# Kernel tuning notes

Hardware: AMD Instinct MI355X
Metric: run time of the kernel (lower is better)

The kernel has to match this reference:

```python
import jax, jax.numpy as jnp
import numpy as np

SQRT_2_OVER_PI = 0.7978845608028654
GELU_COEFF = 0.044715

def _gelu_tanh(v):
    inner = SQRT_2_OVER_PI * (v + GELU_COEFF * v * v * v)
    return 0.5 * v * (1.0 + jnp.tanh(inner))

def setup_inputs() -> dict:
    key = jax.random.key(0)
    k1, k2, k3, k4 = jax.random.split(key, 4)
    M, K, N = 16384, 4096, 4096
    x = jax.random.normal(k1, (M, K), dtype=jnp.float32)
    bound_w = np.sqrt(6.0 / K) / np.sqrt(1.0 + 5.0)  # kaiming_uniform a=sqrt(5)
    weight = jax.random.uniform(k2, (K, N), dtype=jnp.float32, minval=-bound_w, maxval=bound_w)
    bound_b = 1.0 / np.sqrt(K)
    bias = jax.random.uniform(k3, (N,), dtype=jnp.float32, minval=-bound_b, maxval=bound_b)
    subtract = jax.random.normal(k4, (N,), dtype=jnp.float32)
    return {"x": x, "weight": weight, "bias": bias, "subtract": subtract}

def reference(x, weight, bias, subtract):
    # mean_n(xW + b - s) = (x . colsum(W) + sum(b) - sum(s)) / N
    N = weight.shape[1]
    c = weight.sum(axis=1)                       # (K,)
    scale = 1.0 / N
    bias_term = (bias.sum() - subtract.sum()) * scale
    row_scalars = _gelu_tanh(x @ c * scale + bias_term)  # (M,)
    return x + row_scalars[:, None]
```

## Files before the change

### kernel.cpp

```cpp
#include <hip/hip_runtime.h>
#include <math.h>

#define K_DIM 4096
#define N_DIM 4096

__global__ void __launch_bounds__(256) colsum_kernel(const float* __restrict__ W,
                                                     float* __restrict__ c) {
    const int k = blockIdx.x;
    const float4* row = reinterpret_cast<const float4*>(W + (size_t)k * N_DIM);
    const int t = threadIdx.x;
    float acc = 0.f;
#pragma unroll
    for (int i = 0; i < N_DIM / 4 / 256; ++i) {
        float4 v = row[t + i * 256];
        acc += (v.x + v.y) + (v.z + v.w);
    }
#pragma unroll
    for (int off = 32; off > 0; off >>= 1) acc += __shfl_down(acc, off, 64);
    __shared__ float s[4];
    const int wave = t >> 6, lane = t & 63;
    if (lane == 0) s[wave] = acc;
    __syncthreads();
    if (t == 0) c[k] = (s[0] + s[1]) + (s[2] + s[3]);
}

__global__ void __launch_bounds__(256) biassum_kernel(const float* __restrict__ bias,
                                                      const float* __restrict__ subtract,
                                                      float* __restrict__ bterm) {
    const int t = threadIdx.x;
    float acc = 0.f;
    for (int i = t; i < N_DIM; i += 256) acc += bias[i] - subtract[i];
#pragma unroll
    for (int off = 32; off > 0; off >>= 1) acc += __shfl_down(acc, off, 64);
    __shared__ float s[4];
    const int wave = t >> 6, lane = t & 63;
    if (lane == 0) s[wave] = acc;
    __syncthreads();
    if (t == 0) bterm[0] = ((s[0] + s[1]) + (s[2] + s[3])) * (1.0f / (float)N_DIM);
}

__global__ void __launch_bounds__(256) rowfuse_kernel(const float* __restrict__ x,
                                                      const float* __restrict__ c,
                                                      const float* __restrict__ bterm,
                                                      float* __restrict__ out) {
    const int m = blockIdx.x;
    const float4* xr = reinterpret_cast<const float4*>(x + (size_t)m * K_DIM);
    float4* orow = reinterpret_cast<float4*>(out + (size_t)m * K_DIM);
    const float4* c4 = reinterpret_cast<const float4*>(c);
    const int t = threadIdx.x;

    float4 xv[4];
    float acc = 0.f;
#pragma unroll
    for (int i = 0; i < 4; ++i) {
        xv[i] = xr[t + i * 256];
        float4 cv = c4[t + i * 256];
        acc += xv[i].x * cv.x + xv[i].y * cv.y + xv[i].z * cv.z + xv[i].w * cv.w;
    }
#pragma unroll
    for (int off = 32; off > 0; off >>= 1) acc += __shfl_down(acc, off, 64);

    __shared__ float s[4];
    __shared__ float sg;
    const int wave = t >> 6, lane = t & 63;
    if (lane == 0) s[wave] = acc;
    __syncthreads();
    if (t == 0) {
        float d = ((s[0] + s[1]) + (s[2] + s[3])) * (1.0f / (float)N_DIM) + bterm[0];
        float inner = 0.7978845608028654f * (d + 0.044715f * d * d * d);
        sg = 0.5f * d * (1.0f + tanhf(inner));
    }
    __syncthreads();
    const float g = sg;
#pragma unroll
    for (int i = 0; i < 4; ++i) {
        float4 o = xv[i];
        o.x += g; o.y += g; o.z += g; o.w += g;
        orow[t + i * 256] = o;
    }
}

extern "C" void kernel_launch(void* const* d_in, const int* in_sizes, int n_in,
                              void* d_out, int out_size, void* d_ws, size_t ws_size,
                              hipStream_t stream) {
    const float* x        = (const float*)d_in[0];
    const float* W        = (const float*)d_in[1];
    const float* bias     = (const float*)d_in[2];
    const float* subtract = (const float*)d_in[3];
    float* out = (float*)d_out;

    float* c     = (float*)d_ws;
    float* bterm = c + K_DIM;

    const int M = in_sizes[0] / K_DIM;

    colsum_kernel<<<K_DIM, 256, 0, stream>>>(W, c);
    biassum_kernel<<<1, 256, 0, stream>>>(bias, subtract, bterm);
    rowfuse_kernel<<<M, 256, 0, stream>>>(x, c, bterm, out);
}
```

Baseline: 120.3 us.

## Merge bias-sum into colsum kernel and process multiple rows per block with prefetch

Folds the bias/subtract reduction into an extra block of the colsum kernel, which removes one launch. The row kernel now handles 8 rows per block: it loads c once into registers, prefetches the next row's x while reducing the current one, and uses xor shuffles so every thread computes GELU itself, dropping the second barrier. It also swaps tanhf for an exp-based form and writes the output with nontemporal stores. The trade-offs are more register pressure, fewer blocks, and a shared-memory array indexed per row with only one barrier per row, where correctness relies on each row having its own slot.

```diff
diff --git a/kernel.cpp b/kernel.cpp
--- a/kernel.cpp
+++ b/kernel.cpp
@@ -3,80 +3,101 @@
 
 #define K_DIM 4096
 #define N_DIM 4096
+#define ROWS_PER_BLOCK 8
+
+typedef float f32x4 __attribute__((ext_vector_type(4)));
 
 __global__ void __launch_bounds__(256) colsum_kernel(const float* __restrict__ W,
-                                                     float* __restrict__ c) {
-    const int k = blockIdx.x;
-    const float4* row = reinterpret_cast<const float4*>(W + (size_t)k * N_DIM);
+                                                     const float* __restrict__ bias,
+                                                     const float* __restrict__ subtract,
+                                                     float* __restrict__ c,
+                                                     float* __restrict__ bterm) {
     const int t = threadIdx.x;
-    float acc = 0.f;
-#pragma unroll
-    for (int i = 0; i < N_DIM / 4 / 256; ++i) {
-        float4 v = row[t + i * 256];
-        acc += (v.x + v.y) + (v.z + v.w);
-    }
-#pragma unroll
-    for (int off = 32; off > 0; off >>= 1) acc += __shfl_down(acc, off, 64);
     __shared__ float s[4];
     const int wave = t >> 6, lane = t & 63;
-    if (lane == 0) s[wave] = acc;
-    __syncthreads();
-    if (t == 0) c[k] = (s[0] + s[1]) + (s[2] + s[3]);
-}
 
-__global__ void __launch_bounds__(256) biassum_kernel(const float* __restrict__ bias,
-                                                      const float* __restrict__ subtract,
-                                                      float* __restrict__ bterm) {
-    const int t = threadIdx.x;
-    float acc = 0.f;
-    for (int i = t; i < N_DIM; i += 256) acc += bias[i] - subtract[i];
+    if (blockIdx.x < K_DIM) {
+        const int k = blockIdx.x;
+        const float4* row = reinterpret_cast<const float4*>(W + (size_t)k * N_DIM);
+        float acc = 0.f;
 #pragma unroll
-    for (int off = 32; off > 0; off >>= 1) acc += __shfl_down(acc, off, 64);
-    __shared__ float s[4];
-    const int wave = t >> 6, lane = t & 63;
-    if (lane == 0) s[wave] = acc;
-    __syncthreads();
-    if (t == 0) bterm[0] = ((s[0] + s[1]) + (s[2] + s[3])) * (1.0f / (float)N_DIM);
+        for (int i = 0; i < N_DIM / 4 / 256; ++i) {
+            float4 v = row[t + i * 256];
+            acc += (v.x + v.y) + (v.z + v.w);
+        }
+#pragma unroll
+        for (int off = 32; off > 0; off >>= 1) acc += __shfl_down(acc, off, 64);
+        if (lane == 0) s[wave] = acc;
+        __syncthreads();
+        if (t == 0) c[k] = (s[0] + s[1]) + (s[2] + s[3]);
+    } else {
+        float acc = 0.f;
+        for (int i = t; i < N_DIM; i += 256) acc += bias[i] - subtract[i];
+#pragma unroll
+        for (int off = 32; off > 0; off >>= 1) acc += __shfl_down(acc, off, 64);
+        if (lane == 0) s[wave] = acc;
+        __syncthreads();
+        if (t == 0) bterm[0] = ((s[0] + s[1]) + (s[2] + s[3])) * (1.0f / (float)N_DIM);
+    }
 }
 
 __global__ void __launch_bounds__(256) rowfuse_kernel(const float* __restrict__ x,
                                                       const float* __restrict__ c,
                                                       const float* __restrict__ bterm,
-                                                      float* __restrict__ out) {
-    const int m = blockIdx.x;
-    const float4* xr = reinterpret_cast<const float4*>(x + (size_t)m * K_DIM);
-    float4* orow = reinterpret_cast<float4*>(out + (size_t)m * K_DIM);
+                                                      float* __restrict__ out,
+                                                      int M) {
+    const int t = threadIdx.x;
+    const int row0 = blockIdx.x * ROWS_PER_BLOCK;
+
     const float4* c4 = reinterpret_cast<const float4*>(c);
-    const int t = threadIdx.x;
+    float4 cv[4];
+#pragma unroll
+    for (int i = 0; i < 4; ++i) cv[i] = c4[t + i * 256];
+    const float bt = bterm[0];
 
-    float4 xv[4];
-    float acc = 0.f;
+    const float4* xr = reinterpret_cast<const float4*>(x) + (size_t)row0 * (K_DIM / 4);
+    f32x4* orow      = reinterpret_cast<f32x4*>(out)      + (size_t)row0 * (K_DIM / 4);
+
+    __shared__ float s[ROWS_PER_BLOCK][4];
+    const int wave = t >> 6, lane = t & 63;
+
+    float4 xv[2][4];
 #pragma unroll
-    for (int i = 0; i < 4; ++i) {
-        xv[i] = xr[t + i * 256];
-        float4 cv = c4[t + i * 256];
-        acc += xv[i].x * cv.x + xv[i].y * cv.y + xv[i].z * cv.z + xv[i].w * cv.w;
-    }
+    for (int i = 0; i < 4; ++i) xv[0][i] = xr[t + i * 256];
+
 #pragma unroll
-    for (int off = 32; off > 0; off >>= 1) acc += __shfl_down(acc, off, 64);
+    for (int r = 0; r < ROWS_PER_BLOCK; ++r) {
+        const int cur = r & 1, nxt = cur ^ 1;
+        if (r + 1 < ROWS_PER_BLOCK) {
+#pragma unroll
+            for (int i = 0; i < 4; ++i)
+                xv[nxt][i] = xr[(size_t)(r + 1) * (K_DIM / 4) + t + i * 256];
+        }
+        float acc = 0.f;
+#pragma unroll
+        for (int i = 0; i < 4; ++i)
+            acc += xv[cur][i].x * cv[i].x + xv[cur][i].y * cv[i].y
+                 + xv[cur][i].z * cv[i].z + xv[cur][i].w * cv[i].w;
+#pragma unroll
+        for (int off = 32; off > 0; off >>= 1) acc += __shfl_xor(acc, off, 64);
+        if (lane == 0) s[r][wave] = acc;
+        __syncthreads();
 
-    __shared__ float s[4];
-    __shared__ float sg;
-    const int wave = t >> 6, lane = t & 63;
-    if (lane == 0) s[wave] = acc;
-    __syncthreads();
-    if (t == 0) {
-        float d = ((s[0] + s[1]) + (s[2] + s[3])) * (1.0f / (float)N_DIM) + bterm[0];
+        float d = ((s[r][0] + s[r][1]) + (s[r][2] + s[r][3])) * (1.0f / (float)N_DIM) + bt;
         float inner = 0.7978845608028654f * (d + 0.044715f * d * d * d);
-        sg = 0.5f * d * (1.0f + tanhf(inner));
-    }
-    __syncthreads();
-    const float g = sg;
+        float e  = __expf(2.0f * inner);
+        float th = 1.0f - 2.0f / (e + 1.0f);
+        float g  = 0.5f * d * (1.0f + th);
+
 #pragma unroll
-    for (int i = 0; i < 4; ++i) {
-        float4 o = xv[i];
-        o.x += g; o.y += g; o.z += g; o.w += g;
-        orow[t + i * 256] = o;
+        for (int i = 0; i < 4; ++i) {
+            f32x4 o;
+            o.x = xv[cur][i].x + g;
+            o.y = xv[cur][i].y + g;
+            o.z = xv[cur][i].z + g;
+            o.w = xv[cur][i].w + g;
+            __builtin_nontemporal_store(o, &orow[(size_t)r * (K_DIM / 4) + t + i * 256]);
+        }
     }
 }
 
@@ -94,7 +115,6 @@
 
     const int M = in_sizes[0] / K_DIM;
 
-    colsum_kernel<<<K_DIM, 256, 0, stream>>>(W, c);
-    biassum_kernel<<<1, 256, 0, stream>>>(bias, subtract, bterm);
-    rowfuse_kernel<<<M, 256, 0, stream>>>(x, c, bterm, out);
+    colsum_kernel<<<K_DIM + 1, 256, 0, stream>>>(W, bias, subtract, c, bterm);
+    rowfuse_kernel<<<M / ROWS_PER_BLOCK, 256, 0, stream>>>(x, c, bterm, out, M);
 }
```

Result: no change. 122.2 us (+1.6%).

## Merge bias-sum into colsum kernel and process one row per wave

Applied to the files above, without the earlier changes.

The bias/subtract reduction moves into an extra block of the column-sum kernel, which removes one kernel launch. The row kernel now assigns one row per wavefront, so each block covers four rows. This removes the shared-memory reduction and block barriers, and uses xor shuffles so every lane gets the dot product. tanh is computed with a fast exp formula. Each thread now keeps 16 float4 in registers, which may reduce occupancy, and the fast tanh slightly changes precision.

```diff
diff --git a/kernel.cpp b/kernel.cpp
--- a/kernel.cpp
+++ b/kernel.cpp
@@ -3,80 +3,80 @@
 
 #define K_DIM 4096
 #define N_DIM 4096
+#define WAVES_PER_BLOCK 4
 
 __global__ void __launch_bounds__(256) colsum_kernel(const float* __restrict__ W,
-                                                     float* __restrict__ c) {
-    const int k = blockIdx.x;
-    const float4* row = reinterpret_cast<const float4*>(W + (size_t)k * N_DIM);
+                                                     const float* __restrict__ bias,
+                                                     const float* __restrict__ subtract,
+                                                     float* __restrict__ c,
+                                                     float* __restrict__ bterm) {
     const int t = threadIdx.x;
-    float acc = 0.f;
-#pragma unroll
-    for (int i = 0; i < N_DIM / 4 / 256; ++i) {
-        float4 v = row[t + i * 256];
-        acc += (v.x + v.y) + (v.z + v.w);
-    }
-#pragma unroll
-    for (int off = 32; off > 0; off >>= 1) acc += __shfl_down(acc, off, 64);
     __shared__ float s[4];
     const int wave = t >> 6, lane = t & 63;
-    if (lane == 0) s[wave] = acc;
-    __syncthreads();
-    if (t == 0) c[k] = (s[0] + s[1]) + (s[2] + s[3]);
-}
 
-__global__ void __launch_bounds__(256) biassum_kernel(const float* __restrict__ bias,
-                                                      const float* __restrict__ subtract,
-                                                      float* __restrict__ bterm) {
-    const int t = threadIdx.x;
-    float acc = 0.f;
-    for (int i = t; i < N_DIM; i += 256) acc += bias[i] - subtract[i];
+    if (blockIdx.x < K_DIM) {
+        const int k = blockIdx.x;
+        const float4* row = reinterpret_cast<const float4*>(W + (size_t)k * N_DIM);
+        float acc = 0.f;
 #pragma unroll
-    for (int off = 32; off > 0; off >>= 1) acc += __shfl_down(acc, off, 64);
-    __shared__ float s[4];
-    const int wave = t >> 6, lane = t & 63;
-    if (lane == 0) s[wave] = acc;
-    __syncthreads();
-    if (t == 0) bterm[0] = ((s[0] + s[1]) + (s[2] + s[3])) * (1.0f / (float)N_DIM);
+        for (int i = 0; i < N_DIM / 4 / 256; ++i) {
+            float4 v = row[t + i * 256];
+            acc += (v.x + v.y) + (v.z + v.w);
+        }
+#pragma unroll
+        for (int off = 32; off > 0; off >>= 1) acc += __shfl_down(acc, off, 64);
+        if (lane == 0) s[wave] = acc;
+        __syncthreads();
+        if (t == 0) c[k] = (s[0] + s[1]) + (s[2] + s[3]);
+    } else {
+        float acc = 0.f;
+        for (int i = t; i < N_DIM; i += 256) acc += bias[i] - subtract[i];
+#pragma unroll
+        for (int off = 32; off > 0; off >>= 1) acc += __shfl_down(acc, off, 64);
+        if (lane == 0) s[wave] = acc;
+        __syncthreads();
+        if (t == 0) bterm[0] = ((s[0] + s[1]) + (s[2] + s[3])) * (1.0f / (float)N_DIM);
+    }
 }
 
 __global__ void __launch_bounds__(256) rowfuse_kernel(const float* __restrict__ x,
                                                       const float* __restrict__ c,
                                                       const float* __restrict__ bterm,
                                                       float* __restrict__ out) {
-    const int m = blockIdx.x;
-    const float4* xr = reinterpret_cast<const float4*>(x + (size_t)m * K_DIM);
-    float4* orow = reinterpret_cast<float4*>(out + (size_t)m * K_DIM);
+    const int t = threadIdx.x;
+    const int wave = t >> 6, lane = t & 63;
+    const size_t m = (size_t)blockIdx.x * WAVES_PER_BLOCK + wave;
+
+    const float4* xr = reinterpret_cast<const float4*>(x + m * (size_t)K_DIM);
     const float4* c4 = reinterpret_cast<const float4*>(c);
-    const int t = threadIdx.x;
+    float4*       orow = reinterpret_cast<float4*>(out + m * (size_t)K_DIM);
 
-    float4 xv[4];
-    float acc = 0.f;
+    float4 xv[16];
+    float a0 = 0.f, a1 = 0.f, a2 = 0.f, a3 = 0.f;
 #pragma unroll
-    for (int i = 0; i < 4; ++i) {
-        xv[i] = xr[t + i * 256];
-        float4 cv = c4[t + i * 256];
-        acc += xv[i].x * cv.x + xv[i].y * cv.y + xv[i].z * cv.z + xv[i].w * cv.w;
+    for (int i = 0; i < 16; ++i) {
+        xv[i] = xr[lane + i * 64];
+        float4 cvv = c4[lane + i * 64];
+        a0 += xv[i].x * cvv.x;
+        a1 += xv[i].y * cvv.y;
+        a2 += xv[i].z * cvv.z;
+        a3 += xv[i].w * cvv.w;
     }
+    float acc = (a0 + a1) + (a2 + a3);
 #pragma unroll
-    for (int off = 32; off > 0; off >>= 1) acc += __shfl_down(acc, off, 64);
+    for (int off = 32; off > 0; off >>= 1) acc += __shfl_xor(acc, off, 64);
 
-    __shared__ float s[4];
-    __shared__ float sg;
-    const int wave = t >> 6, lane = t & 63;
-    if (lane == 0) s[wave] = acc;
-    __syncthreads();
-    if (t == 0) {
-        float d = ((s[0] + s[1]) + (s[2] + s[3])) * (1.0f / (float)N_DIM) + bterm[0];
-        float inner = 0.7978845608028654f * (d + 0.044715f * d * d * d);
-        sg = 0.5f * d * (1.0f + tanhf(inner));
-    }
-    __syncthreads();
-    const float g = sg;
+    float d = acc * (1.0f / (float)N_DIM) + bterm[0];
+    float inner = 0.7978845608028654f * (d + 0.044715f * d * d * d);
+    float e  = __expf(2.0f * inner);
+    float th = 1.0f - 2.0f / (e + 1.0f);
+    float g  = 0.5f * d * (1.0f + th);
+
 #pragma unroll
-    for (int i = 0; i < 4; ++i) {
+    for (int i = 0; i < 16; ++i) {
         float4 o = xv[i];
         o.x += g; o.y += g; o.z += g; o.w += g;
-        orow[t + i * 256] = o;
+        orow[lane + i * 64] = o;
     }
 }
 
@@ -94,7 +94,6 @@
 
     const int M = in_sizes[0] / K_DIM;
 
-    colsum_kernel<<<K_DIM, 256, 0, stream>>>(W, c);
-    biassum_kernel<<<1, 256, 0, stream>>>(bias, subtract, bterm);
-    rowfuse_kernel<<<M, 256, 0, stream>>>(x, c, bterm, out);
+    colsum_kernel<<<K_DIM + 1, 256, 0, stream>>>(W, bias, subtract, c, bterm);
+    rowfuse_kernel<<<M / WAVES_PER_BLOCK, 256, 0, stream>>>(x, c, bterm, out);
 }
```

Result: slower. 122.9 us (+2.2%).
